# Optimization experiments

Hardware: AMD Instinct MI355X
Metric: run time of the kernel (lower is better)

The kernel has to match this reference:

```python
import jax, jax.numpy as jnp
import numpy as np

NEG = -1e30


def matmul_a_logb(A, B):
    # C = log(A @ exp(B)), stabilized over B's row axis (dim ndim-2)
    bd = B.ndim - 2
    Bm = jnp.max(B, axis=bd, keepdims=True)
    return jnp.log(A @ jnp.exp(B - Bm)) + Bm


def matmul_loga_b(A, B):
    Am = jnp.max(A, axis=-1, keepdims=True)
    return jnp.log(jnp.exp(A - Am) @ B) + Am


def matmul_log(A, B):
    Am = jnp.max(A, axis=-1, keepdims=True)
    Bm = jnp.max(B, axis=-2, keepdims=True)
    return jnp.log(jnp.exp(A - Am) @ jnp.exp(B - Bm)) + Am + Bm


def n2n(x):
    return jnp.nan_to_num(x, neginf=NEG)


def setup_inputs() -> dict:
    H, V, S, E, B, P, L, T = 2048, 32000, 64, 512, 8, 16, 8, 32
    key = jax.random.key(0)
    ks = jax.random.split(key, 11)
    bern = lambda k, sh: jax.random.randint(k, sh, 0, 2).astype(jnp.float32)
    range_mask = bern(ks[7], (B, T + 1)).at[:, -1].set(1.0)  # each range non-empty
    accept_mask = bern(ks[6], (S,)).at[0].set(1.0)           # >=1 accept state
    return {
        'alpha': jax.random.normal(ks[0], (H, H), jnp.float32),
        'beta_raw': jax.random.normal(ks[1], (H, V), jnp.float32),
        'gamma_raw': jax.random.normal(ks[2], (H,), jnp.float32),
        'T_mask': bern(ks[3], (E, V)),
        'VE_mask': bern(ks[4], (S, E)),
        'EV_mask': bern(ks[5], (E, S)),
        'accept_mask': accept_mask,
        'range_mask': range_mask,
        'prefixes': jax.random.randint(ks[8], (B, P), 0, V, jnp.int32),
        'suffix': jax.random.randint(ks[9], (L,), 0, V, jnp.int32),
        'states': jax.random.randint(ks[10], (B,), 0, S, jnp.int32),
    }


def reference(alpha, beta_raw, gamma_raw, T_mask, VE_mask, EV_mask,
              accept_mask, range_mask, prefixes, suffix, states):
    H = alpha.shape[0]
    S = VE_mask.shape[0]
    Bn, Tp1 = range_mask.shape

    alpha_exp = jax.nn.softmax(alpha, axis=1)
    beta = jax.nn.log_softmax(beta_raw, axis=1)       # [H,V]
    gamma = jax.nn.log_softmax(gamma_raw, axis=0)     # [H]

    # --- A cache: forward HMM pass over each prefix ---
    def pref_step(y, tok):
        y = y + beta[:, tok]
        return matmul_loga_b(y[None, :], alpha_exp)[0], None

    def run_prefix(toks):
        y, _ = jax.lax.scan(pref_step, gamma, toks)
        return y

    A = jax.vmap(run_prefix)(prefixes)                # [B,H]

    # --- B cache endpoint: backward HMM pass over suffix ---
    def suf_step(y, tok):
        y = matmul_a_logb(alpha_exp, y[:, None])[:, 0] + beta[:, tok]
        return y, None
    y_suf, _ = jax.lax.scan(suf_step, beta[:, suffix[-1]], suffix[:-1][::-1])

    # --- C cache: DFA-structured recurrence over remaining tokens ---
    T_weights = n2n(matmul_a_logb(T_mask, beta.T))    # [E,H]
    y_ = jnp.where(accept_mask[:, None] > 0, y_suf[None, :], NEG)  # [S,H]
    y0 = matmul_loga_b(y_, alpha_exp.T)

    def c_step(y, _):
        y = n2n(matmul_a_logb(EV_mask, y))            # [E,H]
        y = n2n(matmul_a_logb(VE_mask, T_weights + y))  # [S,H]
        y = matmul_loga_b(y, alpha_exp.T)
        return y, y

    _, Cs = jax.lax.scan(c_step, y0, None, length=Tp1 - 1)
    C = jnp.concatenate([y0[None], Cs], axis=0)       # [T+1,S,H]

    # range aggregation (logsumexp over allowed remaining-length window)
    Cr = n2n(matmul_a_logb(range_mask, C.reshape(Tp1, S * H))).reshape(Bn, S, H)

    # --- compute_logits main batch path ---
    Cfull = A[:, None, :] + Cr                        # [B,S,H]
    logits_pre = matmul_log(Cfull.reshape(Bn * S, H), beta).reshape(Bn, S, -1)  # [B,S,V]

    m3 = VE_mask[states][:, :, None] * EV_mask[None, :, :]   # [B,E,S]
    m = jnp.einsum('bes,ev->bsv', m3, T_mask)                # [B,S,V]
    logmask = n2n(jnp.log(m))

    logits = jax.nn.logsumexp(logits_pre + logmask, axis=1)  # [B,V]
    logits_ = matmul_log(A, beta)                            # [B,V]
    return jnp.stack([logits, logits_], axis=0)              # [2,B,V]
```

## Files before the change

kernel.cpp:

```cpp
#include <hip/hip_runtime.h>
#include <hip/hip_bf16.h>

#define H   2048
#define V   32000
#define SS  64
#define EE  512
#define BB  8
#define PP  16
#define LL  8
#define TT  32
#define TP1 33
#define BSZ 512
#define NEGV -1e30f

typedef unsigned short u16;
typedef unsigned int   u32;
typedef short bf16x8 __attribute__((ext_vector_type(8)));
typedef float f32x4  __attribute__((ext_vector_type(4)));

__device__ __forceinline__ float bf2f(u16 x){ return __uint_as_float(((u32)x) << 16); }
__device__ __forceinline__ u16 f2bf(float f){
  u32 u = __float_as_uint(f);
  return (u16)((u + 0x7fffu + ((u >> 16) & 1u)) >> 16);
}
__device__ __forceinline__ u32 encf(float f){ u32 u = __float_as_uint(f); return (u & 0x80000000u) ? ~u : (u | 0x80000000u); }
__device__ __forceinline__ float decf(u32 e){ u32 u = (e & 0x80000000u) ? (e & 0x7fffffffu) : ~e; return __uint_as_float(u); }

__device__ __forceinline__ int bswz(int n, int kr){
  return ((n*40 + (kr & ~7)) ^ ((n>>1) & 56)) + (kr & 7);
}
__device__ __forceinline__ int bswz_rd(int n, int k8){
  return (n*40 + k8) ^ ((n>>1) & 56);
}

__global__ __launch_bounds__(512) void k_beta(const float* __restrict__ braw, float* __restrict__ rowlse, u16* __restrict__ expB){
  int h = blockIdx.x, t = threadIdx.x;
  __shared__ float red[8];
  __shared__ float red2[8];
  const float* row = braw + (size_t)h * V;
  uint2 stash[16];
  float m = -INFINITY;
  #pragma unroll
  for (int it = 0; it < 16; ++it){
    int idx = (it*512 + t)*4;
    if (idx < V){
      float4 x = *(const float4*)(row + idx);
      u16 b0=f2bf(x.x), b1=f2bf(x.y), b2=f2bf(x.z), b3=f2bf(x.w);
      stash[it] = make_uint2(((u32)b1<<16)|b0, ((u32)b3<<16)|b2);
      m = fmaxf(m, fmaxf(fmaxf(x.x,x.y),fmaxf(x.z,x.w)));
    }
  }
  for (int off=32; off; off>>=1) m = fmaxf(m, __shfl_xor(m, off, 64));
  if ((t&63)==0) red[t>>6] = m;
  __syncthreads();
  m = red[0];
  #pragma unroll
  for (int wv=1; wv<8; ++wv) m = fmaxf(m, red[wv]);
  float s0=0.f, s1=0.f;
  #pragma unroll
  for (int it = 0; it < 16; ++it){
    int idx = (it*512 + t)*4;
    if (idx < V){
      uint2 pk = stash[it];
      float e0 = expf(bf2f((u16)(pk.x      )) - m);
      float e1 = expf(bf2f((u16)(pk.x >> 16)) - m);
      float e2 = expf(bf2f((u16)(pk.y      )) - m);
      float e3 = expf(bf2f((u16)(pk.y >> 16)) - m);
      stash[it] = make_uint2(((u32)f2bf(e1)<<16)|f2bf(e0), ((u32)f2bf(e3)<<16)|f2bf(e2));
      s0 += e0 + e2; s1 += e1 + e3;
    }
  }
  float s = s0 + s1;
  for (int off=32; off; off>>=1) s += __shfl_xor(s, off, 64);
  if ((t&63)==0) red2[t>>6] = s;
  __syncthreads();
  s = (red2[0]+red2[1])+(red2[2]+red2[3])+(red2[4]+red2[5])+(red2[6]+red2[7]);
  if (t == 0) rowlse[h] = m + logf(s);
  float inv = 1.f / s;
  u16* orow = expB + (size_t)h*V;
  #pragma unroll
  for (int it = 0; it < 16; ++it){
    int idx = (it*512 + t)*4;
    if (idx < V){
      uint2 pk = stash[it];
      u16 a0 = f2bf(bf2f((u16)(pk.x      )) * inv);
      u16 a1 = f2bf(bf2f((u16)(pk.x >> 16)) * inv);
      u16 a2 = f2bf(bf2f((u16)(pk.y      )) * inv);
      u16 a3 = f2bf(bf2f((u16)(pk.y >> 16)) * inv);
      *(uint2*)(orow + idx) = make_uint2(((u32)a1<<16)|a0, ((u32)a3<<16)|a2);
    }
  }
}

__global__ __launch_bounds__(256) void k_alpha(const float* __restrict__ a, float* __restrict__ af, u16* __restrict__ abf){
  int r = blockIdx.x, t = threadIdx.x;
  __shared__ float ld[H];
  __shared__ float red[8];
  const float* row = a + (size_t)r * H;
  for (int i=0;i<8;++i){ int j=i*256+t; ld[j]=row[j]; }
  __syncthreads();
  float m=-INFINITY; for(int i=0;i<8;++i) m=fmaxf(m, ld[i*256+t]);
  for(int off=32;off;off>>=1) m=fmaxf(m,__shfl_xor(m,off,64));
  if((t&63)==0) red[t>>6]=m;
  __syncthreads();
  m=fmaxf(fmaxf(red[0],red[1]),fmaxf(red[2],red[3]));
  float s=0.f; for(int i=0;i<8;++i) s+=expf(ld[i*256+t]-m);
  for(int off=32;off;off>>=1) s+=__shfl_xor(s,off,64);
  if((t&63)==0) red[4+(t>>6)]=s;
  __syncthreads();
  s=red[4]+red[5]+red[6]+red[7];
  float inv=1.f/s;
  for(int i=0;i<8;++i){ int j=i*256+t; float e=expf(ld[j]-m)*inv; af[(size_t)r*H+j]=e; abf[(size_t)r*H+j]=f2bf(e); }
}

__global__ __launch_bounds__(256) void k_gamma(const float* __restrict__ graw, float* __restrict__ G){
  int t = threadIdx.x;
  __shared__ float ld[H]; __shared__ float red[8];
  for (int i=0;i<8;++i){ int j=i*256+t; ld[j]=graw[j]; }
  __syncthreads();
  float m=-INFINITY; for(int i=0;i<8;++i) m=fmaxf(m, ld[i*256+t]);
  for(int off=32;off;off>>=1) m=fmaxf(m,__shfl_xor(m,off,64));
  if((t&63)==0) red[t>>6]=m;
  __syncthreads();
  m=fmaxf(fmaxf(red[0],red[1]),fmaxf(red[2],red[3]));
  float s=0.f; for(int i=0;i<8;++i) s+=expf(ld[i*256+t]-m);
  for(int off=32;off;off>>=1) s+=__shfl_xor(s,off,64);
  if((t&63)==0) red[4+(t>>6)]=s;
  __syncthreads();
  s=red[4]+red[5]+red[6]+red[7];
  float lse=m+logf(s);
  for(int i=0;i<8;++i){ int j=i*256+t; G[j]=ld[j]-lse; }
}

__global__ __launch_bounds__(256) void k_prefd(const float* __restrict__ braw, const float* __restrict__ rowlse, const int* __restrict__ pref, float* __restrict__ D){
  int blk = blockIdx.x; int ts = blk >> 3, b = blk & 7; int t = threadIdx.x;
  int tok = pref[b*PP + ts];
  float m = -INFINITY;
  for (int i=0;i<8;++i){ int hh=i*256+t; m = fmaxf(m, braw[(size_t)hh*V + tok] - rowlse[hh]); }
  __shared__ float red[4];
  for(int off=32;off;off>>=1) m=fmaxf(m,__shfl_xor(m,off,64));
  if((t&63)==0) red[t>>6]=m;
  __syncthreads();
  if (t==0) D[ts*BB + b] = fmaxf(fmaxf(red[0],red[1]),fmaxf(red[2],red[3]));
}

__global__ __launch_bounds__(256) void k_mask(const float* __restrict__ EV, const float* __restrict__ VE, u16* __restrict__ EVbf, u16* __restrict__ VEbf){
  int idx = blockIdx.x*256 + threadIdx.x;
  EVbf[idx] = f2bf(EV[idx]);
  VEbf[idx] = f2bf(VE[idx]);
}

__global__ __launch_bounds__(256) void k_cvtT(const float* __restrict__ T, u16* __restrict__ Tbf){
  int i = (blockIdx.x*256 + threadIdx.x)*4;
  float4 x = *(const float4*)(T + i);
  *(uint2*)(Tbf + i) = make_uint2(((u32)f2bf(x.y)<<16)|f2bf(x.x), ((u32)f2bf(x.w)<<16)|f2bf(x.z));
}

__global__ __launch_bounds__(256) void k_a3(const float* __restrict__ VE, const float* __restrict__ EV, const int* __restrict__ states, u16* __restrict__ A3){
  int idx = blockIdx.x*256 + threadIdx.x;
  int bs = idx >> 9, e = idx & 511;
  int b = bs >> 6, s = bs & 63;
  A3[idx] = f2bf(VE[states[b]*EE + e] * EV[e*SS + s]);
}

__global__ __launch_bounds__(256) void k_ascan(const float* __restrict__ braw, const float* __restrict__ rowlse,
    const float* __restrict__ alpha_f, const float* __restrict__ G, const float* __restrict__ D,
    const int* __restrict__ pref, float* __restrict__ PA, u32* __restrict__ MAXPA, float* __restrict__ MUA, int tstep){
  int bid = blockIdx.x; int kc = bid & 31, jt = bid >> 5; int t = threadIdx.x;
  __shared__ float ey[BB][64];
  __shared__ float wred[4][BB];
  const float* PAprev = PA + (size_t)(tstep-1)*BB*H;
  float* PAcur = PA + (size_t)tstep*BB*H;
  for (int i = 0; i < 2; ++i){
    int idx = i*256 + t; int b = idx >> 6, hl = idx & 63; int hh = kc*64 + hl;
    int tok = pref[b*PP + (tstep-1)];
    float bcol = braw[(size_t)hh*V + tok] - rowlse[hh];
    float Db = D[(tstep-1)*BB + b];
    float v;
    if (tstep == 1){
      v = expf(G[hh] + bcol - Db);
    } else {
      float p = PAprev[b*H + hh];
      float mp = fmaxf(__uint_as_float(MAXPA[(tstep-1)*BB + b]), 1e-30f);
      v = p > 0.f ? p * (1.f/mp) * expf(bcol - Db) : 0.f;
    }
    ey[b][hl] = v;
  }
  __syncthreads();
  int j = jt*256 + t;
  float acc[BB];
  #pragma unroll
  for (int b=0;b<BB;++b) acc[b]=0.f;
  for (int hl = 0; hl < 64; ++hl){
    float a = alpha_f[(size_t)(kc*64 + hl)*H + j];
    #pragma unroll
    for (int b=0;b<BB;++b) acc[b] += ey[b][hl] * a;
  }
  #pragma unroll
  for (int b=0;b<BB;++b){
    atomicAdd(&PAcur[b*H + j], acc[b]);
    float mv = acc[b];
    for (int off=32;off;off>>=1) mv = fmaxf(mv, __shfl_xor(mv, off, 64));
    if ((t&63)==0) wred[t>>6][b] = mv;
  }
  __syncthreads();
  if (t < BB){
    float mv = fmaxf(fmaxf(wred[0][t],wred[1][t]),fmaxf(wred[2][t],wred[3][t]));
    atomicMax(&MAXPA[tstep*BB + t], __float_as_uint(fmaxf(mv, 0.f)));
  }
  if (bid == 0 && t < BB){
    float mu = MUA[(tstep-1)*BB + t];
    if (tstep > 1) mu += logf(fmaxf(__uint_as_float(MAXPA[(tstep-1)*BB + t]), 1e-30f));
    MUA[tstep*BB + t] = mu + D[(tstep-1)*BB + t];
  }
}

__global__ __launch_bounds__(256) void k_suffix(const float* __restrict__ braw, const float* __restrict__ rowlse,
    const float* __restrict__ alpha_f, const int* __restrict__ suffix, float* __restrict__ YS, int step){
  int t = threadIdx.x, blk = blockIdx.x;
  __shared__ float ye[H]; __shared__ float red[4];
  const float* src = YS + (step & 1)*H;
  float* dst = YS + (1 - (step & 1))*H;
  int tok_in = suffix[LL-1];
  for (int i=0;i<8;++i){
    int jj = i*256 + t;
    ye[jj] = (step == 0) ? (braw[(size_t)jj*V + tok_in] - rowlse[jj]) : src[jj];
  }
  __syncthreads();
  float m=-INFINITY;
  for(int i=0;i<8;++i) m=fmaxf(m, ye[i*256+t]);
  for(int off=32;off;off>>=1) m=fmaxf(m,__shfl_xor(m,off,64));
  if((t&63)==0) red[t>>6]=m;
  __syncthreads();
  m=fmaxf(fmaxf(red[0],red[1]),fmaxf(red[2],red[3]));
  for (int i=0;i<8;++i){ int jj=i*256+t; ye[jj] = expf(ye[jj]-m); }
  __syncthreads();
  int w = t >> 6, lane = t & 63;
  int r = blk*4 + w;
  float acc = 0.f;
  for (int k2=0;k2<32;++k2){ int jj=k2*64+lane; acc += alpha_f[(size_t)r*H + jj]*ye[jj]; }
  for(int off=32;off;off>>=1) acc += __shfl_xor(acc,off,64);
  if (lane==0){
    int tok = suffix[LL-2-step];
    dst[r] = logf(acc) + m + (braw[(size_t)r*V + tok] - rowlse[r]);
  }
}

__global__ __launch_bounds__(256) void k_c0(const float* __restrict__ YS, const float* __restrict__ accept, float* __restrict__ Y2T, u32* __restrict__ MU2){
  int blk = blockIdx.x, t = threadIdx.x;
  const float* ysuf = YS + H;
  int h0 = blk*32;
  for (int i=0;i<8;++i){
    int idx = i*256 + t; int r = idx >> 6, s = idx & 63;
    Y2T[(size_t)(h0+r)*SS + s] = accept[s] > 0.f ? ysuf[h0 + r] : NEGV;
  }
  if (blk == 0){
    __shared__ float red[4];
    float m=-INFINITY;
    for(int i=0;i<8;++i) m = fmaxf(m, ysuf[i*256+t]);
    for(int off=32;off;off>>=1) m=fmaxf(m,__shfl_xor(m,off,64));
    if((t&63)==0) red[t>>6]=m;
    __syncthreads();
    if (t < SS){
      float mm = fmaxf(fmaxf(red[0],red[1]),fmaxf(red[2],red[3]));
      MU2[t] = encf(accept[t] > 0.f ? mm : NEGV);
    }
  }
}

__global__ __launch_bounds__(256) void k_pgemm(const u16* __restrict__ abf, const float* __restrict__ Y2T, const u32* __restrict__ MU2t, float* __restrict__ PTt){
  int bid = blockIdx.x; int kc = bid & 15, mt = bid >> 4; int t = threadIdx.x;
  __shared__ u16 Alds[128*40];
  __shared__ u16 Blds[64*40];
  __shared__ float muld[SS];
  if (t < SS) muld[t] = decf(MU2t[t]);
  __syncthreads();
  int m0 = mt*128;
  int w = t >> 6, lane = t & 63, l15 = lane & 15, q = lane >> 4;
  f32x4 acc[2][4];
  for(int a=0;a<2;++a)for(int b=0;b<4;++b)for(int c=0;c<4;++c) acc[a][b][c]=0.f;
  for (int it=0; it<4; ++it){
    int kb = kc*128 + it*32;
    { int row = t >> 1, cg = (t & 1)*16;
      const u16* src = abf + (size_t)(m0+row)*H + kb + cg;
      *(uint4*)&Alds[row*40+cg]   = *(const uint4*)src;
      *(uint4*)&Alds[row*40+cg+8] = *(const uint4*)(src+8);
    }
    for (int i=0;i<8;++i){
      int idx = i*256 + t; int kr = idx >> 6, s = idx & 63;
      float y = Y2T[(size_t)(kb+kr)*SS + s];
      Blds[bswz(s, kr)] = f2bf(expf(y - muld[s]));
    }
    __syncthreads();
    bf16x8 bv[4];
    #pragma unroll
    for (int nf=0; nf<4; ++nf){ int nn = nf*16 + l15; bv[nf] = *(bf16x8*)&Blds[bswz_rd(nn, q*8)]; }
    #pragma unroll
    for (int mf=0; mf<2; ++mf){
      bf16x8 a = *(bf16x8*)&Alds[(w*32 + mf*16 + l15)*40 + q*8];
      #pragma unroll
      for (int nf=0; nf<4; ++nf)
        acc[mf][nf] = __builtin_amdgcn_mfma_f32_16x16x32_bf16(a, bv[nf], acc[mf][nf], 0, 0, 0);
    }
    __syncthreads();
  }
  #pragma unroll
  for (int mf=0;mf<2;++mf)
  #pragma unroll
  for (int nf=0;nf<4;++nf)
  #pragma unroll
  for (int reg=0;reg<4;++reg){
    int j = m0 + w*32 + mf*16 + q*4 + reg;
    int s = nf*16 + l15;
    atomicAdd(&PTt[(size_t)j*SS + s], acc[mf][nf][reg]);
  }
}

__global__ __launch_bounds__(256) void k_cstep(const float* __restrict__ PTprev, const u32* __restrict__ MU2prev,
    const float* __restrict__ TwT, const u16* __restrict__ EVbf, const u16* __restrict__ VEbf,
    float* __restrict__ Y2T, u32* __restrict__ MU2t){
  int blk = blockIdx.x, t = threadIdx.x;
  int h0 = blk*16;
  __shared__ float ytile[16*64];
  __shared__ float muprev[SS];
  __shared__ float mx[16];
  __shared__ u32 mzenc[16];
  __shared__ float mzf[16];
  __shared__ u16 EYl[16*72];
  __shared__ u16 EZl[16*520];
  if (t < SS) muprev[t] = decf(MU2prev[t]);
  if (t >= 64 && t < 80) mzenc[t-64] = 0u;
  __syncthreads();
  for (int i=0;i<4;++i){
    int idx = i*256 + t; int r = idx >> 6, s = idx & 63;
    float p = PTprev[(size_t)(h0+r)*SS + s];
    ytile[r*64+s] = (p > 0.f) ? (logf(p) + muprev[s]) : NEGV;
  }
  __syncthreads();
  { int r = t >> 4, i4 = t & 15;
    float m = ytile[r*64 + i4*4];
    m = fmaxf(m, ytile[r*64 + i4*4 + 1]);
    m = fmaxf(m, ytile[r*64 + i4*4 + 2]);
    m = fmaxf(m, ytile[r*64 + i4*4 + 3]);
    for (int d=1; d<16; d<<=1) m = fmaxf(m, __shfl_xor(m, d, 64));
    if (i4 == 0) mx[r] = m;
  }
  __syncthreads();
  for (int i=0;i<4;++i){
    int idx = i*256 + t; int r = idx >> 6, s = idx & 63;
    EYl[r*72 + s] = f2bf(expf(ytile[r*64+s] - mx[r]));
  }
  __syncthreads();
  int w = t >> 6, lane = t & 63, l15 = lane & 15, q = lane >> 4;
  f32x4 acc1[8];
  for (int nf=0;nf<8;++nf) for(int c=0;c<4;++c) acc1[nf][c]=0.f;
  #pragma unroll
  for (int kf=0; kf<2; ++kf){
    bf16x8 a = *(bf16x8*)&EYl[l15*72 + kf*32 + q*8];
    #pragma unroll
    for (int nf=0; nf<8; ++nf){
      int e = w*128 + nf*16 + l15;
      bf16x8 b = *(const bf16x8*)&EVbf[(size_t)e*SS + kf*32 + q*8];
      acc1[nf] = __builtin_amdgcn_mfma_f32_16x16x32_bf16(a, b, acc1[nf], 0, 0, 0);
    }
  }
  #pragma unroll
  for (int nf=0; nf<8; ++nf){
    int e = w*128 + nf*16 + l15;
    #pragma unroll
    for (int reg=0; reg<4; ++reg){
      int r = q*4 + reg;
      float S1 = acc1[nf][reg];
      acc1[nf][reg] = (S1 > 0.f ? (logf(S1) + mx[r]) : NEGV) + TwT[(size_t)(h0+r)*EE + e];
    }
  }
  #pragma unroll
  for (int reg=0; reg<4; ++reg){
    float zm = acc1[0][reg];
    #pragma unroll
    for (int nf=1; nf<8; ++nf) zm = fmaxf(zm, acc1[nf][reg]);
    for (int d=1; d<16; d<<=1) zm = fmaxf(zm, __shfl_xor(zm, d, 64));
    if (l15 == 0) atomicMax(&mzenc[q*4 + reg], encf(zm));
  }
  __syncthreads();
  if (t < 16) mzf[t] = decf(mzenc[t]);
  __syncthreads();
  #pragma unroll
  for (int nf=0; nf<8; ++nf){
    int e = w*128 + nf*16 + l15;
    #pragma unroll
    for (int reg=0; reg<4; ++reg){
      int r = q*4 + reg;
      EZl[r*520 + e] = f2bf(expf(acc1[nf][reg] - mzf[r]));
    }
  }
  __syncthreads();
  f32x4 acc2;
  for(int c=0;c<4;++c) acc2[c]=0.f;
  #pragma unroll
  for (int kc2=0; kc2<16; ++kc2){
    bf16x8 a = *(bf16x8*)&EZl[l15*520 + kc2*32 + q*8];
    bf16x8 b = *(const bf16x8*)&VEbf[(size_t)(w*16 + l15)*EE + kc2*32 + q*8];
    acc2 = __builtin_amdgcn_mfma_f32_16x16x32_bf16(a, b, acc2, 0, 0, 0);
  }
  int s = w*16 + l15;
  float cm = -INFINITY;
  #pragma unroll
  for (int reg=0; reg<4; ++reg){
    int r = q*4 + reg;
    float S2 = acc2[reg];
    float y2 = S2 > 0.f ? (logf(S2) + mzf[r]) : NEGV;
    Y2T[(size_t)(h0+r)*SS + s] = y2;
    cm = fmaxf(cm, y2);
  }
  cm = fmaxf(cm, __shfl_xor(cm, 16, 64));
  cm = fmaxf(cm, __shfl_xor(cm, 32, 64));
  if (q == 0) atomicMax(&MU2t[s], encf(cm));
}

__global__ __launch_bounds__(256) void k_twgemm(const u16* __restrict__ Abf, const u16* __restrict__ Bbf, float* __restrict__ Cacc){
  int bid = blockIdx.x; int t = threadIdx.x;
  int kc = bid % 10; int rest = bid / 10;
  int nt = rest & 3; int mt = rest >> 2;
  int m0 = mt*128, n0 = nt*128;
  __shared__ u16 Alds[128*40];
  __shared__ u16 Blds[128*40];
  int w = t>>6, lane = t&63, l15 = lane&15, q = lane>>4;
  int wm = w >> 1, wn = w & 1;
  f32x4 acc[4][4];
  for(int a=0;a<4;++a)for(int b=0;b<4;++b)for(int c=0;c<4;++c)acc[a][b][c]=0.f;
  for (int it=0; it<100; ++it){
    int kb = (kc*100 + it)*32;
    { int row = t>>1, cg = (t&1)*16;
      const u16* srcA = Abf + (size_t)(m0+row)*V + kb + cg;
      *(uint4*)&Alds[row*40+cg]   = *(const uint4*)srcA;
      *(uint4*)&Alds[row*40+cg+8] = *(const uint4*)(srcA+8);
      const u16* srcB = Bbf + (size_t)(n0+row)*V + kb + cg;
      *(uint4*)&Blds[row*40+cg]   = *(const uint4*)srcB;
      *(uint4*)&Blds[row*40+cg+8] = *(const uint4*)(srcB+8);
    }
    __syncthreads();
    bf16x8 av[4], bv[4];
    #pragma unroll
    for (int mf=0;mf<4;++mf) av[mf] = *(bf16x8*)&Alds[(wm*64+mf*16+l15)*40 + q*8];
    #pragma unroll
    for (int nf=0;nf<4;++nf) bv[nf] = *(bf16x8*)&Blds[(wn*64+nf*16+l15)*40 + q*8];
    #pragma unroll
    for (int mf=0;mf<4;++mf)
      #pragma unroll
      for (int nf=0;nf<4;++nf)
        acc[mf][nf] = __builtin_amdgcn_mfma_f32_16x16x32_bf16(av[mf], bv[nf], acc[mf][nf], 0, 0, 0);
    __syncthreads();
  }
  #pragma unroll
  for (int mf=0;mf<4;++mf)
  #pragma unroll
  for (int nf=0;nf<4;++nf)
  #pragma unroll
  for (int reg=0;reg<4;++reg){
    int m = m0 + wm*64 + mf*16 + q*4 + reg;
    int n = n0 + wn*64 + nf*16 + l15;
    atomicAdd(&Cacc[(size_t)m*EE + n], acc[mf][nf][reg]);
  }
}

__global__ __launch_bounds__(256) void k_twlog(float* __restrict__ TwT){
  int idx = blockIdx.x*256 + threadIdx.x;
  float v = TwT[idx];
  TwT[idx] = v > 0.f ? logf(v) : NEGV;
}

__global__ __launch_bounds__(256) void k_range(const float* __restrict__ PT, const u32* __restrict__ MU2,
    const float* __restrict__ rmask, const float* __restrict__ PA, const float* __restrict__ MUA,
    float* __restrict__ Cfull, u32* __restrict__ M1e){
  int blk = blockIdx.x, t = threadIdx.x; int h0 = blk*16;
  __shared__ float muf[TP1*SS];
  __shared__ float rm[BB*TP1];
  __shared__ float muA[BB];
  for (int i = t; i < TP1*SS; i += 256) muf[i] = decf(MU2[i]);
  for (int i = t; i < BB*TP1; i += 256) rm[i] = rmask[i];
  if (t < BB) muA[t] = MUA[16*BB + t];
  __syncthreads();
  const float* PA16 = PA + (size_t)16*BB*H;
  int s = t & 63; int hb = t >> 6;
  float tmax[BB];
  #pragma unroll
  for (int b=0;b<BB;++b) tmax[b] = -INFINITY;
  for (int i=0;i<4;++i){
    int h = h0 + hb*4 + i;
    float c[TP1];
    float M = -INFINITY;
    #pragma unroll
    for (int tt=0; tt<TP1; ++tt){
      float p = PT[(size_t)tt*(H*SS) + (size_t)h*SS + s];
      float cv = p > 0.f ? (logf(p) + muf[tt*SS + s]) : NEGV;
      c[tt] = cv; M = fmaxf(M, cv);
    }
    #pragma unroll
    for (int tt=0; tt<TP1; ++tt) c[tt] = expf(c[tt] - M);
    #pragma unroll
    for (int b=0;b<BB;++b){
      float a = 0.f;
      #pragma unroll
      for (int tt=0; tt<TP1; ++tt) a += rm[b*TP1 + tt]*c[tt];
      float cr = a > 0.f ? (logf(a) + M) : NEGV;
      float pa = PA16[b*H + h];
      float Ab = pa > 0.f ? (logf(pa) + muA[b]) : NEGV;
      float cf = Ab + cr;
      Cfull[((size_t)(b*SS + s))*H + h] = cf;
      tmax[b] = fmaxf(tmax[b], cf);
    }
  }
  #pragma unroll
  for (int b=0;b<BB;++b) atomicMax(&M1e[b*SS + s], encf(tmax[b]));
}

__global__ void k_mb(const u32* __restrict__ M1e, float* __restrict__ W, float* __restrict__ MB){
  int t = threadIdx.x;
  float m1 = decf(M1e[t]);
  float m = m1;
  for (int off=32; off; off>>=1) m = fmaxf(m, __shfl_xor(m, off, 64));
  if ((t&63)==0) MB[t>>6] = m;
  W[t] = expf(m1 - m);
}

__global__ __launch_bounds__(256) void k_expcf(const float* __restrict__ Cfull, const u32* __restrict__ M1e, u16* __restrict__ expCf){
  int idx = blockIdx.x*256 + threadIdx.x;
  int bs = idx >> 11;
  expCf[idx] = f2bf(expf(Cfull[idx] - decf(M1e[bs])));
}

__global__ __launch_bounds__(256) void k_expa(const float* __restrict__ PA, const float* __restrict__ MUA, u16* __restrict__ expA, float* __restrict__ maxA){
  int b = blockIdx.x, t = threadIdx.x;
  const float* PA16 = PA + (size_t)16*BB*H + (size_t)b*H;
  __shared__ float al[H]; __shared__ float red[4];
  float mua = MUA[16*BB + b];
  for (int i=0;i<8;++i){ int h=i*256+t; float p=PA16[h]; al[h] = p>0.f ? (logf(p)+mua) : NEGV; }
  __syncthreads();
  float m=-INFINITY; for(int i=0;i<8;++i) m=fmaxf(m, al[i*256+t]);
  for(int off=32;off;off>>=1) m=fmaxf(m,__shfl_xor(m,off,64));
  if((t&63)==0) red[t>>6]=m;
  __syncthreads();
  m=fmaxf(fmaxf(red[0],red[1]),fmaxf(red[2],red[3]));
  if (t==0) maxA[b]=m;
  for (int i=0;i<8;++i){ int h=i*256+t; expA[b*H+h]=f2bf(expf(al[h]-m)); }
}

__global__ __launch_bounds__(256) void k_flog(const u16* __restrict__ expCf, const u16* __restrict__ expB,
    const u16* __restrict__ A3, const u16* __restrict__ Tbf,
    const float* __restrict__ W, const float* __restrict__ MB, float* __restrict__ out){
  int bid = blockIdx.x; int t = threadIdx.x;
  int nt = bid % 250, mt = bid / 250;
  int m0 = mt*128, n0 = nt*128;
  __shared__ u16 Alds[128*40];
  __shared__ u16 Blds[128*40];
  __shared__ float Wl[BSZ];
  for (int i=t; i<BSZ; i+=256) Wl[i] = W[i];
  int w = t>>6, lane = t&63, l15 = lane&15, q = lane>>4;
  int wm = w >> 1, wn = w & 1;
  f32x4 acc[4][4];
  for(int a=0;a<4;++a)for(int b=0;b<4;++b)for(int c=0;c<4;++c)acc[a][b][c]=0.f;
  for (int it=0; it<16; ++it){
    int kb = it*32;
    { int row = t>>1, cg = (t&1)*16;
      const u16* src = A3 + (size_t)(m0+row)*EE + kb + cg;
      *(uint4*)&Alds[row*40+cg]   = *(const uint4*)src;
      *(uint4*)&Alds[row*40+cg+8] = *(const uint4*)(src+8);
    }
    { int kr = t>>3, ng = (t&7)*16;
      const u16* src = Tbf + (size_t)(kb+kr)*V + n0 + ng;
      uint4 x0 = *(const uint4*)src;
      uint4 x1 = *(const uint4*)(src + 8);
      const u16* px = (const u16*)&x0;
      const u16* py = (const u16*)&x1;
      #pragma unroll
      for (int jj=0; jj<8; ++jj) Blds[bswz(ng+jj, kr)] = px[jj];
      #pragma unroll
      for (int jj=0; jj<8; ++jj) Blds[bswz(ng+8+jj, kr)] = py[jj];
    }
    __syncthreads();
    bf16x8 av[4], bv[4];
    #pragma unroll
    for (int mf=0;mf<4;++mf) av[mf] = *(bf16x8*)&Alds[(wm*64+mf*16+l15)*40 + q*8];
    #pragma unroll
    for (int nf=0;nf<4;++nf){ int nn = wn*64+nf*16+l15; bv[nf] = *(bf16x8*)&Blds[bswz_rd(nn, q*8)]; }
    #pragma unroll
    for (int mf=0;mf<4;++mf)
      #pragma unroll
      for (int nf=0;nf<4;++nf)
        acc[mf][nf] = __builtin_amdgcn_mfma_f32_16x16x32_bf16(av[mf], bv[nf], acc[mf][nf], 0, 0, 0);
    __syncthreads();
  }
  float s2[4][4][4];
  #pragma unroll
  for (int mf=0;mf<4;++mf)
  #pragma unroll
  for (int nf=0;nf<4;++nf)
  #pragma unroll
  for (int reg=0;reg<4;++reg){ s2[mf][nf][reg] = acc[mf][nf][reg]; acc[mf][nf][reg] = 0.f; }
  for (int it=0; it<64; ++it){
    int kb = it*32;
    { int row = t>>1, cg = (t&1)*16;
      const u16* src = expCf + (size_t)(m0+row)*H + kb + cg;
      *(uint4*)&Alds[row*40+cg]   = *(const uint4*)src;
      *(uint4*)&Alds[row*40+cg+8] = *(const uint4*)(src+8);
    }
    { int kr = t>>3, ng = (t&7)*16;
      const u16* src = expB + (size_t)(kb+kr)*V + n0 + ng;
      uint4 x0 = *(const uint4*)src;
      uint4 x1 = *(const uint4*)(src + 8);
      const u16* px = (const u16*)&x0;
      const u16* py = (const u16*)&x1;
      #pragma unroll
      for (int jj=0; jj<8; ++jj) Blds[bswz(ng+jj, kr)] = px[jj];
      #pragma unroll
      for (int jj=0; jj<8; ++jj) Blds[bswz(ng+8+jj, kr)] = py[jj];
    }
    __syncthreads();
    bf16x8 av[4], bv[4];
    #pragma unroll
    for (int mf=0;mf<4;++mf) av[mf] = *(bf16x8*)&Alds[(wm*64+mf*16+l15)*40 + q*8];
    #pragma unroll
    for (int nf=0;nf<4;++nf){ int nn = wn*64+nf*16+l15; bv[nf] = *(bf16x8*)&Blds[bswz_rd(nn, q*8)]; }
    #pragma unroll
    for (int mf=0;mf<4;++mf)
      #pragma unroll
      for (int nf=0;nf<4;++nf)
        acc[mf][nf] = __builtin_amdgcn_mfma_f32_16x16x32_bf16(av[mf], bv[nf], acc[mf][nf], 0, 0, 0);
    __syncthreads();
  }
  int b = mt*2 + wm;
  float mb = MB[b];
  #pragma unroll
  for (int nf=0; nf<4; ++nf){
    float v = 0.f;
    #pragma unroll
    for (int mf=0; mf<4; ++mf)
      #pragma unroll
      for (int reg=0; reg<4; ++reg)
        v += acc[mf][nf][reg] * s2[mf][nf][reg] * Wl[m0 + wm*64 + mf*16 + q*4 + reg];
    v += __shfl_xor(v, 16, 64);
    v += __shfl_xor(v, 32, 64);
    if (q == 0){
      int n = n0 + wn*64 + nf*16 + l15;
      out[(size_t)b*V + n] = v > 0.f ? (logf(v) + mb) : NEGV;
    }
  }
}

__global__ __launch_bounds__(256) void k_lg2(const u16* __restrict__ expA, const u16* __restrict__ expB, float* __restrict__ S_){
  int bid = blockIdx.x; int kc = bid & 7, vt = bid >> 3; int t = threadIdx.x;
  int v = vt*256 + t; int hh0 = kc*256;
  __shared__ float ea[BB][256];
  for (int i=0;i<8;++i){ int idx=i*256+t; int b=idx>>8, hl=idx&255; ea[b][hl]=bf2f(expA[b*H + hh0 + hl]); }
  __syncthreads();
  float acc[BB];
  #pragma unroll
  for(int b=0;b<BB;++b)acc[b]=0.f;
  for (int hl=0; hl<256; ++hl){
    float ex = bf2f(expB[(size_t)(hh0+hl)*V + v]);
    #pragma unroll
    for(int b=0;b<BB;++b) acc[b] += ea[b][hl]*ex;
  }
  #pragma unroll
  for(int b=0;b<BB;++b) atomicAdd(&S_[b*V + v], acc[b]);
}

__global__ __launch_bounds__(256) void k_lfin(const float* __restrict__ S_, const float* __restrict__ maxA, float* __restrict__ out){
  int idx = blockIdx.x*256 + threadIdx.x;
  int b = idx / V;
  float sv = S_[idx];
  out[BB*V + idx] = sv > 0.f ? (logf(sv) + maxA[b]) : NEGV;
}

extern "C" void kernel_launch(void* const* d_in, const int* in_sizes, int n_in,
                              void* d_out, int out_size, void* d_ws, size_t ws_size,
                              hipStream_t stream){
  (void)in_sizes; (void)n_in; (void)out_size; (void)ws_size;
  const float* alpha_in  = (const float*)d_in[0];
  const float* beta_raw  = (const float*)d_in[1];
  const float* gamma_raw = (const float*)d_in[2];
  const float* T_mask    = (const float*)d_in[3];
  const float* VE_mask   = (const float*)d_in[4];
  const float* EV_mask   = (const float*)d_in[5];
  const float* accept    = (const float*)d_in[6];
  const float* rmask     = (const float*)d_in[7];
  const int* prefixes    = (const int*)d_in[8];
  const int* suffix      = (const int*)d_in[9];
  const int* states      = (const int*)d_in[10];
  float* out = (float*)d_out;

  char* base = (char*)d_ws;
  size_t off = 0;
  auto alloc = [&](size_t bytes)->char*{ char* r = base + off; off = (off + bytes + 255) & ~(size_t)255; return r; };
  float* PT    = (float*)alloc((size_t)TP1*H*SS*4);
  float* PA    = (float*)alloc((size_t)17*BB*H*4);
  u32*   MAXPA = (u32*)  alloc(17*BB*4);
  float* MUA   = (float*)alloc(17*BB*4);
  u32*   MU2   = (u32*)  alloc(TP1*SS*4);
  float* TwT   = (float*)alloc((size_t)H*EE*4);
  u32*   M1e   = (u32*)  alloc(BSZ*4);
  float* S_    = (float*)alloc((size_t)BB*V*4);
  size_t zero_end = off;
  float* alpha_f  = (float*)alloc((size_t)H*H*4);
  u16*   alpha_bf = (u16*)  alloc((size_t)H*H*2);
  float* rowlse   = (float*)alloc(H*4);
  float* G        = (float*)alloc(H*4);
  float* D        = (float*)alloc(PP*BB*4);
  float* YS       = (float*)alloc(2*H*4);
  u16*   EVbf     = (u16*)  alloc(EE*SS*2);
  u16*   VEbf     = (u16*)  alloc(SS*EE*2);
  float* Y2T      = (float*)alloc((size_t)H*SS*4);
  u16*   expB     = (u16*)  alloc((size_t)H*V*2);
  u16*   Tbf      = (u16*)  alloc((size_t)EE*V*2);
  float* Cfull    = (float*)alloc((size_t)BSZ*H*4);
  u16*   expCf    = (u16*)  alloc((size_t)BSZ*H*2);
  u16*   expA     = (u16*)  alloc(BB*H*2);
  float* maxA     = (float*)alloc(BB*4);
  u16*   A3       = (u16*)  alloc((size_t)BSZ*EE*2);
  float* W        = (float*)alloc(BSZ*4);
  float* MB       = (float*)alloc(BB*4);

  hipMemsetAsync(d_ws, 0, zero_end, stream);

  k_beta <<<H, 512, 0, stream>>>(beta_raw, rowlse, expB);
  k_alpha<<<H, 256, 0, stream>>>(alpha_in, alpha_f, alpha_bf);
  k_gamma<<<1, 256, 0, stream>>>(gamma_raw, G);
  k_prefd<<<PP*BB, 256, 0, stream>>>(beta_raw, rowlse, prefixes, D);
  k_mask <<<128, 256, 0, stream>>>(EV_mask, VE_mask, EVbf, VEbf);
  k_cvtT <<<EE*V/1024, 256, 0, stream>>>(T_mask, Tbf);
  k_a3   <<<1024, 256, 0, stream>>>(VE_mask, EV_mask, states, A3);

  for (int t = 1; t <= PP; ++t)
    k_ascan<<<256, 256, 0, stream>>>(beta_raw, rowlse, alpha_f, G, D, prefixes, PA, MAXPA, MUA, t);
  for (int i = 0; i < LL-1; ++i)
    k_suffix<<<512, 256, 0, stream>>>(beta_raw, rowlse, alpha_f, suffix, YS, i);

  k_twgemm<<<640, 256, 0, stream>>>(expB, Tbf, TwT);
  k_twlog<<<H*EE/256, 256, 0, stream>>>(TwT);

  k_c0   <<<64, 256, 0, stream>>>(YS, accept, Y2T, MU2);
  k_pgemm<<<256, 256, 0, stream>>>(alpha_bf, Y2T, MU2, PT);
  for (int t = 1; t <= TT; ++t){
    k_cstep<<<128, 256, 0, stream>>>(PT + (size_t)(t-1)*H*SS, MU2 + (t-1)*SS, TwT, EVbf, VEbf, Y2T, MU2 + t*SS);
    k_pgemm<<<256, 256, 0, stream>>>(alpha_bf, Y2T, MU2 + t*SS, PT + (size_t)t*H*SS);
  }

  k_range<<<128, 256, 0, stream>>>(PT, MU2, rmask, PA, MUA, Cfull, M1e);
  k_mb   <<<1, 512, 0, stream>>>(M1e, W, MB);
  k_expcf<<<BSZ*H/256, 256, 0, stream>>>(Cfull, M1e, expCf);
  k_expa <<<BB, 256, 0, stream>>>(PA, MUA, expA, maxA);

  k_flog<<<1000, 256, 0, stream>>>(expCf, expB, A3, Tbf, W, MB, out);

  k_lg2 <<<125*8, 256, 0, stream>>>(expA, expB, S_);
  k_lfin<<<BB*V/256, 256, 0, stream>>>(S_, maxA, out);
}
```

Measured before the change: 2.061 ms.

## Fuse sequential scan launches into persistent kernels with grid barriers

Replaces the per-step launches of the prefix scan, the suffix scan and the C-step/pgemm loop with three persistent kernels that loop over the steps internally. Steps are separated by a software grid barrier built on atomics. This removes roughly eighty small kernel launches and their gaps. In exchange, every block must be co-resident for the spin barrier to avoid deadlock, and the suffix kernel now uses half as many blocks, each doing twice the rows.

```diff
diff --git a/kernel.cpp b/kernel.cpp
--- a/kernel.cpp
+++ b/kernel.cpp
@@ -33,6 +33,20 @@
   return (n*40 + k8) ^ ((n>>1) & 56);
 }
 
+__device__ __forceinline__ void gridbar(u32* bar, u32 target){
+  __syncthreads();
+  if (threadIdx.x == 0){
+    __threadfence();
+    atomicAdd(bar, 1u);
+    for (int spin = 0; spin < (1<<24); ++spin){
+      if (atomicAdd(bar, 0u) >= target) break;
+      __builtin_amdgcn_s_sleep(1);
+    }
+  }
+  __syncthreads();
+  __threadfence();
+}
+
 __global__ __launch_bounds__(512) void k_beta(const float* __restrict__ braw, float* __restrict__ rowlse, u16* __restrict__ expB){
   int h = blockIdx.x, t = threadIdx.x;
   __shared__ float red[8];
@@ -163,86 +177,97 @@
   A3[idx] = f2bf(VE[states[b]*EE + e] * EV[e*SS + s]);
 }
 
-__global__ __launch_bounds__(256) void k_ascan(const float* __restrict__ braw, const float* __restrict__ rowlse,
+__global__ __launch_bounds__(256) void k_ascan_all(const float* __restrict__ braw, const float* __restrict__ rowlse,
     const float* __restrict__ alpha_f, const float* __restrict__ G, const float* __restrict__ D,
-    const int* __restrict__ pref, float* __restrict__ PA, u32* __restrict__ MAXPA, float* __restrict__ MUA, int tstep){
+    const int* __restrict__ pref, float* __restrict__ PA, u32* __restrict__ MAXPA, float* __restrict__ MUA,
+    u32* __restrict__ bar){
   int bid = blockIdx.x; int kc = bid & 31, jt = bid >> 5; int t = threadIdx.x;
   __shared__ float ey[BB][64];
   __shared__ float wred[4][BB];
-  const float* PAprev = PA + (size_t)(tstep-1)*BB*H;
-  float* PAcur = PA + (size_t)tstep*BB*H;
-  for (int i = 0; i < 2; ++i){
-    int idx = i*256 + t; int b = idx >> 6, hl = idx & 63; int hh = kc*64 + hl;
-    int tok = pref[b*PP + (tstep-1)];
-    float bcol = braw[(size_t)hh*V + tok] - rowlse[hh];
-    float Db = D[(tstep-1)*BB + b];
-    float v;
-    if (tstep == 1){
-      v = expf(G[hh] + bcol - Db);
-    } else {
-      float p = PAprev[b*H + hh];
-      float mp = fmaxf(__uint_as_float(MAXPA[(tstep-1)*BB + b]), 1e-30f);
-      v = p > 0.f ? p * (1.f/mp) * expf(bcol - Db) : 0.f;
-    }
-    ey[b][hl] = v;
-  }
-  __syncthreads();
-  int j = jt*256 + t;
-  float acc[BB];
-  #pragma unroll
-  for (int b=0;b<BB;++b) acc[b]=0.f;
-  for (int hl = 0; hl < 64; ++hl){
-    float a = alpha_f[(size_t)(kc*64 + hl)*H + j];
-    #pragma unroll
-    for (int b=0;b<BB;++b) acc[b] += ey[b][hl] * a;
-  }
-  #pragma unroll
-  for (int b=0;b<BB;++b){
-    atomicAdd(&PAcur[b*H + j], acc[b]);
-    float mv = acc[b];
-    for (int off=32;off;off>>=1) mv = fmaxf(mv, __shfl_xor(mv, off, 64));
-    if ((t&63)==0) wred[t>>6][b] = mv;
-  }
-  __syncthreads();
-  if (t < BB){
-    float mv = fmaxf(fmaxf(wred[0][t],wred[1][t]),fmaxf(wred[2][t],wred[3][t]));
-    atomicMax(&MAXPA[tstep*BB + t], __float_as_uint(fmaxf(mv, 0.f)));
-  }
-  if (bid == 0 && t < BB){
-    float mu = MUA[(tstep-1)*BB + t];
-    if (tstep > 1) mu += logf(fmaxf(__uint_as_float(MAXPA[(tstep-1)*BB + t]), 1e-30f));
-    MUA[tstep*BB + t] = mu + D[(tstep-1)*BB + t];
-  }
-}
-
-__global__ __launch_bounds__(256) void k_suffix(const float* __restrict__ braw, const float* __restrict__ rowlse,
-    const float* __restrict__ alpha_f, const int* __restrict__ suffix, float* __restrict__ YS, int step){
+  u32 nb = 0;
+  for (int ts = 1; ts <= PP; ++ts){
+    const float* PAprev = PA + (size_t)(ts-1)*BB*H;
+    float* PAcur = PA + (size_t)ts*BB*H;
+    for (int i = 0; i < 2; ++i){
+      int idx = i*256 + t; int b = idx >> 6, hl = idx & 63; int hh = kc*64 + hl;
+      int tok = pref[b*PP + (ts-1)];
+      float bcol = braw[(size_t)hh*V + tok] - rowlse[hh];
+      float Db = D[(ts-1)*BB + b];
+      float v;
+      if (ts == 1){
+        v = expf(G[hh] + bcol - Db);
+      } else {
+        float p = PAprev[b*H + hh];
+        float mp = fmaxf(__uint_as_float(MAXPA[(ts-1)*BB + b]), 1e-30f);
+        v = p > 0.f ? p * (1.f/mp) * expf(bcol - Db) : 0.f;
+      }
+      ey[b][hl] = v;
+    }
+    __syncthreads();
+    int j = jt*256 + t;
+    float acc[BB];
+    #pragma unroll
+    for (int b=0;b<BB;++b) acc[b]=0.f;
+    for (int hl = 0; hl < 64; ++hl){
+      float a = alpha_f[(size_t)(kc*64 + hl)*H + j];
+      #pragma unroll
+      for (int b=0;b<BB;++b) acc[b] += ey[b][hl] * a;
+    }
+    #pragma unroll
+    for (int b=0;b<BB;++b){
+      atomicAdd(&PAcur[b*H + j], acc[b]);
+      float mv = acc[b];
+      for (int off=32;off;off>>=1) mv = fmaxf(mv, __shfl_xor(mv, off, 64));
+      if ((t&63)==0) wred[t>>6][b] = mv;
+    }
+    __syncthreads();
+    if (t < BB){
+      float mv = fmaxf(fmaxf(wred[0][t],wred[1][t]),fmaxf(wred[2][t],wred[3][t]));
+      atomicMax(&MAXPA[ts*BB + t], __float_as_uint(fmaxf(mv, 0.f)));
+    }
+    if (bid == 0 && t < BB){
+      float mu = MUA[(ts-1)*BB + t];
+      if (ts > 1) mu += logf(fmaxf(__uint_as_float(MAXPA[(ts-1)*BB + t]), 1e-30f));
+      MUA[ts*BB + t] = mu + D[(ts-1)*BB + t];
+    }
+    ++nb; gridbar(bar, 256u*nb);
+  }
+}
+
+__global__ __launch_bounds__(256) void k_sufall(const float* __restrict__ braw, const float* __restrict__ rowlse,
+    const float* __restrict__ alpha_f, const int* __restrict__ suffix, float* __restrict__ YS,
+    u32* __restrict__ bar){
   int t = threadIdx.x, blk = blockIdx.x;
   __shared__ float ye[H]; __shared__ float red[4];
-  const float* src = YS + (step & 1)*H;
-  float* dst = YS + (1 - (step & 1))*H;
   int tok_in = suffix[LL-1];
-  for (int i=0;i<8;++i){
-    int jj = i*256 + t;
-    ye[jj] = (step == 0) ? (braw[(size_t)jj*V + tok_in] - rowlse[jj]) : src[jj];
-  }
-  __syncthreads();
-  float m=-INFINITY;
-  for(int i=0;i<8;++i) m=fmaxf(m, ye[i*256+t]);
-  for(int off=32;off;off>>=1) m=fmaxf(m,__shfl_xor(m,off,64));
-  if((t&63)==0) red[t>>6]=m;
-  __syncthreads();
-  m=fmaxf(fmaxf(red[0],red[1]),fmaxf(red[2],red[3]));
-  for (int i=0;i<8;++i){ int jj=i*256+t; ye[jj] = expf(ye[jj]-m); }
-  __syncthreads();
-  int w = t >> 6, lane = t & 63;
-  int r = blk*4 + w;
-  float acc = 0.f;
-  for (int k2=0;k2<32;++k2){ int jj=k2*64+lane; acc += alpha_f[(size_t)r*H + jj]*ye[jj]; }
-  for(int off=32;off;off>>=1) acc += __shfl_xor(acc,off,64);
-  if (lane==0){
+  u32 nb = 0;
+  for (int step = 0; step < LL-1; ++step){
+    const float* src = YS + (step & 1)*H;
+    float* dst = YS + (1 - (step & 1))*H;
+    for (int i=0;i<8;++i){
+      int jj = i*256 + t;
+      ye[jj] = (step == 0) ? (braw[(size_t)jj*V + tok_in] - rowlse[jj]) : src[jj];
+    }
+    __syncthreads();
+    float m=-INFINITY;
+    for(int i=0;i<8;++i) m=fmaxf(m, ye[i*256+t]);
+    for(int off=32;off;off>>=1) m=fmaxf(m,__shfl_xor(m,off,64));
+    if((t&63)==0) red[t>>6]=m;
+    __syncthreads();
+    m=fmaxf(fmaxf(red[0],red[1]),fmaxf(red[2],red[3]));
+    for (int i=0;i<8;++i){ int jj=i*256+t; ye[jj] = expf(ye[jj]-m); }
+    __syncthreads();
+    int w = t >> 6, lane = t & 63;
     int tok = suffix[LL-2-step];
-    dst[r] = logf(acc) + m + (braw[(size_t)r*V + tok] - rowlse[r]);
+    #pragma unroll
+    for (int sub = 0; sub < 2; ++sub){
+      int r = blk*8 + w*2 + sub;
+      float acc = 0.f;
+      for (int k2=0;k2<32;++k2){ int jj=k2*64+lane; acc += alpha_f[(size_t)r*H + jj]*ye[jj]; }
+      for(int off=32;off;off>>=1) acc += __shfl_xor(acc,off,64);
+      if (lane==0) dst[r] = logf(acc) + m + (braw[(size_t)r*V + tok] - rowlse[r]);
+    }
+    ++nb; gridbar(bar, 256u*nb);
   }
 }
 
@@ -268,11 +293,10 @@
   }
 }
 
-__global__ __launch_bounds__(256) void k_pgemm(const u16* __restrict__ abf, const float* __restrict__ Y2T, const u32* __restrict__ MU2t, float* __restrict__ PTt){
-  int bid = blockIdx.x; int kc = bid & 15, mt = bid >> 4; int t = threadIdx.x;
-  __shared__ u16 Alds[128*40];
-  __shared__ u16 Blds[64*40];
-  __shared__ float muld[SS];
+__device__ __forceinline__ void pgemm_body(int bid, int t, const u16* __restrict__ abf,
+    const float* __restrict__ Y2T, const u32* __restrict__ MU2t, float* __restrict__ PTt,
+    u16* Alds, u16* Blds, float* muld){
+  int kc = bid & 15, mt = bid >> 4;
   if (t < SS) muld[t] = decf(MU2t[t]);
   __syncthreads();
   int m0 = mt*128;
@@ -281,10 +305,10 @@
   for(int a=0;a<2;++a)for(int b=0;b<4;++b)for(int c=0;c<4;++c) acc[a][b][c]=0.f;
   for (int it=0; it<4; ++it){
     int kb = kc*128 + it*32;
-    { int row = t >> 1, cg = (t & 1)*16;
-      const u16* src = abf + (size_t)(m0+row)*H + kb + cg;
-      *(uint4*)&Alds[row*40+cg]   = *(const uint4*)src;
-      *(uint4*)&Alds[row*40+cg+8] = *(const uint4*)(src+8);
+    { int row = t >> 1, cg_ = (t & 1)*16;
+      const u16* src = abf + (size_t)(m0+row)*H + kb + cg_;
+      *(uint4*)&Alds[row*40+cg_]   = *(const uint4*)src;
+      *(uint4*)&Alds[row*40+cg_+8] = *(const uint4*)(src+8);
     }
     for (int i=0;i<8;++i){
       int idx = i*256 + t; int kr = idx >> 6, s = idx & 63;
@@ -316,11 +340,105 @@
   }
 }
 
-__global__ __launch_bounds__(256) void k_cstep(const float* __restrict__ PTprev, const u32* __restrict__ MU2prev,
-    const float* __restrict__ TwT, const u16* __restrict__ EVbf, const u16* __restrict__ VEbf,
-    float* __restrict__ Y2T, u32* __restrict__ MU2t){
+__device__ __forceinline__ void cstep_body(int blk, int t, const float* __restrict__ PTprev,
+    const u32* __restrict__ MU2prev, const float* __restrict__ TwT, const u16* __restrict__ EVbf,
+    const u16* __restrict__ VEbf, float* __restrict__ Y2T, u32* __restrict__ MU2t,
+    float* ytile, float* muprev, float* mx, u32* mzenc, float* mzf, u16* EYl, u16* EZl){
+  int h0 = blk*16;
+  if (t < SS) muprev[t] = decf(MU2prev[t]);
+  if (t >= 64 && t < 80) mzenc[t-64] = 0u;
+  __syncthreads();
+  for (int i=0;i<4;++i){
+    int idx = i*256 + t; int r = idx >> 6, s = idx & 63;
+    float p = PTprev[(size_t)(h0+r)*SS + s];
+    ytile[r*64+s] = (p > 0.f) ? (logf(p) + muprev[s]) : NEGV;
+  }
+  __syncthreads();
+  { int r = t >> 4, i4 = t & 15;
+    float m = ytile[r*64 + i4*4];
+    m = fmaxf(m, ytile[r*64 + i4*4 + 1]);
+    m = fmaxf(m, ytile[r*64 + i4*4 + 2]);
+    m = fmaxf(m, ytile[r*64 + i4*4 + 3]);
+    for (int d=1; d<16; d<<=1) m = fmaxf(m, __shfl_xor(m, d, 64));
+    if (i4 == 0) mx[r] = m;
+  }
+  __syncthreads();
+  for (int i=0;i<4;++i){
+    int idx = i*256 + t; int r = idx >> 6, s = idx & 63;
+    EYl[r*72 + s] = f2bf(expf(ytile[r*64+s] - mx[r]));
+  }
+  __syncthreads();
+  int w = t >> 6, lane = t & 63, l15 = lane & 15, q = lane >> 4;
+  f32x4 acc1[8];
+  for (int nf=0;nf<8;++nf) for(int c=0;c<4;++c) acc1[nf][c]=0.f;
+  #pragma unroll
+  for (int kf=0; kf<2; ++kf){
+    bf16x8 a = *(bf16x8*)&EYl[l15*72 + kf*32 + q*8];
+    #pragma unroll
+    for (int nf=0; nf<8; ++nf){
+      int e = w*128 + nf*16 + l15;
+      bf16x8 b = *(const bf16x8*)&EVbf[(size_t)e*SS + kf*32 + q*8];
+      acc1[nf] = __builtin_amdgcn_mfma_f32_16x16x32_bf16(a, b, acc1[nf], 0, 0, 0);
+    }
+  }
+  #pragma unroll
+  for (int nf=0; nf<8; ++nf){
+    int e = w*128 + nf*16 + l15;
+    #pragma unroll
+    for (int reg=0; reg<4; ++reg){
+      int r = q*4 + reg;
+      float S1 = acc1[nf][reg];
+      acc1[nf][reg] = (S1 > 0.f ? (logf(S1) + mx[r]) : NEGV) + TwT[(size_t)(h0+r)*EE + e];
+    }
+  }
+  #pragma unroll
+  for (int reg=0; reg<4; ++reg){
+    float zm = acc1[0][reg];
+    #pragma unroll
+    for (int nf=1; nf<8; ++nf) zm = fmaxf(zm, acc1[nf][reg]);
+    for (int d=1; d<16; d<<=1) zm = fmaxf(zm, __shfl_xor(zm, d, 64));
+    if (l15 == 0) atomicMax(&mzenc[q*4 + reg], encf(zm));
+  }
+  __syncthreads();
+  if (t < 16) mzf[t] = decf(mzenc[t]);
+  __syncthreads();
+  #pragma unroll
+  for (int nf=0; nf<8; ++nf){
+    int e = w*128 + nf*16 + l15;
+    #pragma unroll
+    for (int reg=0; reg<4; ++reg){
+      int r = q*4 + reg;
+      EZl[r*520 + e] = f2bf(expf(acc1[nf][reg] - mzf[r]));
+    }
+  }
+  __syncthreads();
+  f32x4 acc2;
+  for(int c=0;c<4;++c) acc2[c]=0.f;
+  #pragma unroll
+  for (int kc2=0; kc2<16; ++kc2){
+    bf16x8 a = *(bf16x8*)&EZl[l15*520 + kc2*32 + q*8];
+    bf16x8 b = *(const bf16x8*)&VEbf[(size_t)(w*16 + l15)*EE + kc2*32 + q*8];
+    acc2 = __builtin_amdgcn_mfma_f32_16x16x32_bf16(a, b, acc2, 0, 0, 0);
+  }
+  int s = w*16 + l15;
+  float cm = -INFINITY;
+  #pragma unroll
+  for (int reg=0; reg<4; ++reg){
+    int r = q*4 + reg;
+    float S2 = acc2[reg];
+    float y2 = S2 > 0.f ? (logf(S2) + mzf[r]) : NEGV;
+    Y2T[(size_t)(h0+r)*SS + s] = y2;
+    cm = fmaxf(cm, y2);
+  }
+  cm = fmaxf(cm, __shfl_xor(cm, 16, 64));
+  cm = fmaxf(cm, __shfl_xor(cm, 32, 64));
+  if (q == 0) atomicMax(&MU2t[s], encf(cm));
+}
+
+__global__ __launch_bounds__(256) void k_scan(const u16* __restrict__ abf, float* __restrict__ PT,
+    u32* __restrict__ MU2, float* __restrict__ Y2T, const float* __restrict__ TwT,
+    const u16* __restrict__ EVbf, const u16* __restrict__ VEbf, u32* __restrict__ bar){
   int blk = blockIdx.x, t = threadIdx.x;
-  int h0 = blk*16;
   __shared__ float ytile[16*64];
   __shared__ float muprev[SS];
   __shared__ float mx[16];
@@ -328,94 +446,20 @@
   __shared__ float mzf[16];
   __shared__ u16 EYl[16*72];
   __shared__ u16 EZl[16*520];
-  if (t < SS) muprev[t] = decf(MU2prev[t]);
-  if (t >= 64 && t < 80) mzenc[t-64] = 0u;
-  __syncthreads();
-  for (int i=0;i<4;++i){
-    int idx = i*256 + t; int r = idx >> 6, s = idx & 63;
-    float p = PTprev[(size_t)(h0+r)*SS + s];
-    ytile[r*64+s] = (p > 0.f) ? (logf(p) + muprev[s]) : NEGV;
-  }
-  __syncthreads();
-  { int r = t >> 4, i4 = t & 15;
-    float m = ytile[r*64 + i4*4];
-    m = fmaxf(m, ytile[r*64 + i4*4 + 1]);
-    m = fmaxf(m, ytile[r*64 + i4*4 + 2]);
-    m = fmaxf(m, ytile[r*64 + i4*4 + 3]);
-    for (int d=1; d<16; d<<=1) m = fmaxf(m, __shfl_xor(m, d, 64));
-    if (i4 == 0) mx[r] = m;
-  }
-  __syncthreads();
-  for (int i=0;i<4;++i){
-    int idx = i*256 + t; int r = idx >> 6, s = idx & 63;
-    EYl[r*72 + s] = f2bf(expf(ytile[r*64+s] - mx[r]));
-  }
-  __syncthreads();
-  int w = t >> 6, lane = t & 63, l15 = lane & 15, q = lane >> 4;
-  f32x4 acc1[8];
-  for (int nf=0;nf<8;++nf) for(int c=0;c<4;++c) acc1[nf][c]=0.f;
-  #pragma unroll
-  for (int kf=0; kf<2; ++kf){
-    bf16x8 a = *(bf16x8*)&EYl[l15*72 + kf*32 + q*8];
-    #pragma unroll
-    for (int nf=0; nf<8; ++nf){
-      int e = w*128 + nf*16 + l15;
-      bf16x8 b = *(const bf16x8*)&EVbf[(size_t)e*SS + kf*32 + q*8];
-      acc1[nf] = __builtin_amdgcn_mfma_f32_16x16x32_bf16(a, b, acc1[nf], 0, 0, 0);
-    }
-  }
-  #pragma unroll
-  for (int nf=0; nf<8; ++nf){
-    int e = w*128 + nf*16 + l15;
-    #pragma unroll
-    for (int reg=0; reg<4; ++reg){
-      int r = q*4 + reg;
-      float S1 = acc1[nf][reg];
-      acc1[nf][reg] = (S1 > 0.f ? (logf(S1) + mx[r]) : NEGV) + TwT[(size_t)(h0+r)*EE + e];
-    }
-  }
-  #pragma unroll
-  for (int reg=0; reg<4; ++reg){
-    float zm = acc1[0][reg];
-    #pragma unroll
-    for (int nf=1; nf<8; ++nf) zm = fmaxf(zm, acc1[nf][reg]);
-    for (int d=1; d<16; d<<=1) zm = fmaxf(zm, __shfl_xor(zm, d, 64));
-    if (l15 == 0) atomicMax(&mzenc[q*4 + reg], encf(zm));
-  }
-  __syncthreads();
-  if (t < 16) mzf[t] = decf(mzenc[t]);
-  __syncthreads();
-  #pragma unroll
-  for (int nf=0; nf<8; ++nf){
-    int e = w*128 + nf*16 + l15;
-    #pragma unroll
-    for (int reg=0; reg<4; ++reg){
-      int r = q*4 + reg;
-      EZl[r*520 + e] = f2bf(expf(acc1[nf][reg] - mzf[r]));
-    }
-  }
-  __syncthreads();
-  f32x4 acc2;
-  for(int c=0;c<4;++c) acc2[c]=0.f;
-  #pragma unroll
-  for (int kc2=0; kc2<16; ++kc2){
-    bf16x8 a = *(bf16x8*)&EZl[l15*520 + kc2*32 + q*8];
-    bf16x8 b = *(const bf16x8*)&VEbf[(size_t)(w*16 + l15)*EE + kc2*32 + q*8];
-    acc2 = __builtin_amdgcn_mfma_f32_16x16x32_bf16(a, b, acc2, 0, 0, 0);
-  }
-  int s = w*16 + l15;
-  float cm = -INFINITY;
-  #pragma unroll
-  for (int reg=0; reg<4; ++reg){
-    int r = q*4 + reg;
-    float S2 = acc2[reg];
-    float y2 = S2 > 0.f ? (logf(S2) + mzf[r]) : NEGV;
-    Y2T[(size_t)(h0+r)*SS + s] = y2;
-    cm = fmaxf(cm, y2);
-  }
-  cm = fmaxf(cm, __shfl_xor(cm, 16, 64));
-  cm = fmaxf(cm, __shfl_xor(cm, 32, 64));
-  if (q == 0) atomicMax(&MU2t[s], encf(cm));
+  __shared__ u16 Alds[128*40];
+  __shared__ u16 Bl2[64*40];
+  __shared__ float muld[SS];
+  u32 nb = 0;
+  for (int ts = 0; ts <= TT; ++ts){
+    if (ts > 0){
+      if (blk < 128)
+        cstep_body(blk, t, PT + (size_t)(ts-1)*H*SS, MU2 + (size_t)(ts-1)*SS, TwT, EVbf, VEbf,
+                   Y2T, MU2 + (size_t)ts*SS, ytile, muprev, mx, mzenc, mzf, EYl, EZl);
+      ++nb; gridbar(bar, 256u*nb);
+    }
+    pgemm_body(blk, t, abf, Y2T, MU2 + (size_t)ts*SS, PT + (size_t)ts*H*SS, Alds, Bl2, muld);
+    ++nb; gridbar(bar, 256u*nb);
+  }
 }
 
 __global__ __launch_bounds__(256) void k_twgemm(const u16* __restrict__ Abf, const u16* __restrict__ Bbf, float* __restrict__ Cacc){
@@ -701,6 +745,9 @@
   float* TwT   = (float*)alloc((size_t)H*EE*4);
   u32*   M1e   = (u32*)  alloc(BSZ*4);
   float* S_    = (float*)alloc((size_t)BB*V*4);
+  u32*   BAR0  = (u32*)  alloc(256);
+  u32*   BAR1  = (u32*)  alloc(256);
+  u32*   BAR2  = (u32*)  alloc(256);
   size_t zero_end = off;
   float* alpha_f  = (float*)alloc((size_t)H*H*4);
   u16*   alpha_bf = (u16*)  alloc((size_t)H*H*2);
@@ -731,20 +778,14 @@
   k_cvtT <<<EE*V/1024, 256, 0, stream>>>(T_mask, Tbf);
   k_a3   <<<1024, 256, 0, stream>>>(VE_mask, EV_mask, states, A3);
 
-  for (int t = 1; t <= PP; ++t)
-    k_ascan<<<256, 256, 0, stream>>>(beta_raw, rowlse, alpha_f, G, D, prefixes, PA, MAXPA, MUA, t);
-  for (int i = 0; i < LL-1; ++i)
-    k_suffix<<<512, 256, 0, stream>>>(beta_raw, rowlse, alpha_f, suffix, YS, i);
+  k_ascan_all<<<256, 256, 0, stream>>>(beta_raw, rowlse, alpha_f, G, D, prefixes, PA, MAXPA, MUA, BAR0);
+  k_sufall<<<256, 256, 0, stream>>>(beta_raw, rowlse, alpha_f, suffix, YS, BAR1);
 
   k_twgemm<<<640, 256, 0, stream>>>(expB, Tbf, TwT);
   k_twlog<<<H*EE/256, 256, 0, stream>>>(TwT);
 
   k_c0   <<<64, 256, 0, stream>>>(YS, accept, Y2T, MU2);
-  k_pgemm<<<256, 256, 0, stream>>>(alpha_bf, Y2T, MU2, PT);
-  for (int t = 1; t <= TT; ++t){
-    k_cstep<<<128, 256, 0, stream>>>(PT + (size_t)(t-1)*H*SS, MU2 + (t-1)*SS, TwT, EVbf, VEbf, Y2T, MU2 + t*SS);
-    k_pgemm<<<256, 256, 0, stream>>>(alpha_bf, Y2T, MU2 + t*SS, PT + (size_t)t*H*SS);
-  }
+  k_scan <<<256, 256, 0, stream>>>(alpha_bf, PT, MU2, Y2T, TwT, EVbf, VEbf, BAR2);
 
   k_range<<<128, 256, 0, stream>>>(PT, MU2, rmask, PA, MUA, Cfull, M1e);
   k_mb   <<<1, 512, 0, stream>>>(M1e, W, MB);
```

Measured after the change: 4.078 ms. +97.9%, slower.
